# Kernel optimization log

Measured on AMD Instinct MI355X. Metric: run time of the kernel, lower is better.

The kernel has to match this reference:

```python
import jax, jax.numpy as jnp
import numpy as np

STRIDE = 2
PADDING = 1


def setup_inputs() -> dict:
    key = jax.random.key(0)
    k1, k2, k3, k4, k5 = jax.random.split(key, 5)
    B, C, H, W = 32, 128, 64, 64
    O, kh, kw = 256, 3, 3
    ah = H + 2 * PADDING - (kh - 1)  # 64
    oh = ah // STRIDE                # 32 (divisible -> ceil == floor, rest == 0)
    inputs = {
        "input": jax.random.normal(k1, (B, C, H, W), dtype=jnp.float32),
        "weight": jax.random.normal(k2, (O, C, kh, kw), dtype=jnp.float32) * 0.05,
        "bias": jax.random.normal(k3, (O,), dtype=jnp.float32) * 0.05,
        "selh": jax.random.randint(k4, (oh, oh), 0, STRIDE, dtype=jnp.int32),
        "selw": jax.random.randint(k5, (oh, oh), 0, STRIDE, dtype=jnp.int32),
    }
    return inputs


def reference(input, weight, bias, selh, selw):
    # Faithful to SConv2dAvg.forward with stoch=True, mask == -1, stride=2:
    # unfold(input, k, pad, stride=1) -> stochastic gather of one position per
    # stride x stride cell (offsets selh/selw) -> GEMM with flattened weight -> reshape.
    B, C, H, W = input.shape
    O, _, kh, kw = weight.shape
    ah = H + 2 * PADDING - (kh - 1)
    aw = W + 2 * PADDING - (kw - 1)
    oh = ah // STRIDE  # divisible by construction; ceil_mode correction is a no-op
    ow = aw // STRIDE
    xp = jnp.pad(input, ((0, 0), (0, 0), (PADDING, PADDING), (PADDING, PADDING)))
    # selected unfold positions in the afterconv grid
    rng_h = selh + (jnp.arange(oh, dtype=selh.dtype) * STRIDE)[:, None]   # [oh, ow]
    rng_w = selw + (jnp.arange(ow, dtype=selw.dtype) * STRIDE)[None, :]   # [oh, ow]
    # gather k x k patches directly (equivalent to gathering unfold columns)
    rows = rng_h[:, :, None, None] + jnp.arange(kh)[None, None, :, None]  # [oh, ow, kh, 1]
    cols = rng_w[:, :, None, None] + jnp.arange(kw)[None, None, None, :]  # [oh, ow, 1, kw]
    patches = xp[:, :, rows, cols]  # [B, C, oh, ow, kh, kw]
    out = jnp.einsum('bchwij,ocij->bohw', patches, weight) + bias[None, :, None, None]
    return out  # [B, O, oh, ow]
```

## Files before the change

### kernel.cpp

```cpp
#include <hip/hip_runtime.h>
#include <hip/hip_bf16.h>


typedef short bf16x8 __attribute__((ext_vector_type(8)));
typedef float f32x4  __attribute__((ext_vector_type(4)));

#define NSTEP 36
#define WPRE_BYTES (NSTEP * 256 * 32 * 2)
#define TRANS_BYTES (32 * 66 * 66 * 128 * 2)
#define TOTAL_WS (WPRE_BYTES + TRANS_BYTES)

__device__ __forceinline__ unsigned short f2bf(float x) {
  unsigned u = __float_as_uint(x);
  return (unsigned short)((u + 0x7fffu + ((u >> 16) & 1u)) >> 16);
}
__device__ __forceinline__ unsigned pk2(float a, float b) {
  unsigned ua = __float_as_uint(a), ub = __float_as_uint(b);
  return ((ua + 0x7fffu + ((ua >> 16) & 1u)) >> 16) |
         ((ub + 0x7fffu + ((ub >> 16) & 1u)) & 0xffff0000u);
}
__device__ __forceinline__ bf16x8 ld_frag(const uint4* a) {
  union { uint4 u; bf16x8 s; } cv; cv.u = *a; return cv.s;
}
__device__ __forceinline__ void async16(const void* g, void* l) {
  __builtin_amdgcn_global_load_lds(
      (__attribute__((address_space(1))) void*)(void*)g,
      (__attribute__((address_space(3))) void*)l, 16, 0, 0);
}

__global__ __launch_bounds__(256) void prep(const float* __restrict__ in,
                                            const float* __restrict__ w,
                                            unsigned short* __restrict__ tp,
                                            unsigned short* __restrict__ wpre) {
  const int tid = threadIdx.x;
  if (blockIdx.x >= 66) {
    const int s    = blockIdx.x - 66;
    const int o    = (blockIdx.y << 3) + (tid >> 5);
    const int k_in = tid & 31;
    const int kg   = (s << 5) + (((k_in >> 3) ^ ((o >> 1) & 3)) << 3) + (k_in & 7);
    const int tap  = kg >> 7;
    const int c    = kg & 127;
    const int di   = (tap >= 6) ? 2 : ((tap >= 3) ? 1 : 0);
    const int dj   = tap - di * 3;
    wpre[(s << 13) + (o << 5) + k_in] = f2bf(w[(o * 128 + c) * 9 + di * 3 + dj]);
    return;
  }
  __shared__ float lds[128 * 65];
  const int hp = blockIdx.x;
  const int b  = blockIdx.y;
  uint4* rowp = (uint4*)(tp + (size_t)(b * 66 + hp) * 66 * 128);
  uint4 z; z.x = z.y = z.z = z.w = 0u;
  if (hp == 0 || hp == 65) {
    for (int s = tid; s < 1056; s += 256) rowp[s] = z;
    return;
  }
  const int h = hp - 1;
  const float* src = in + ((size_t)b << 19) + (h << 6);
  const int ww4 = (tid & 15) << 2;
  const int c0  = tid >> 4;
#pragma unroll
  for (int pass = 0; pass < 8; ++pass) {
    int c = (pass << 4) + c0;
    float4 v = *(const float4*)(src + ((size_t)c << 12) + ww4);
    float* lp = lds + c * 65 + ww4;
    lp[0] = v.x; lp[1] = v.y; lp[2] = v.z; lp[3] = v.w;
  }
  __syncthreads();
  for (int s = tid; s < 1056; s += 256) {
    if (s < 16 || s >= 1040) { rowp[s] = z; continue; }
    int idx = s - 16;
    int wq = idx >> 4, c8 = idx & 15;
    const float* lp = lds + (c8 << 3) * 65 + wq;
    uint4 d;
    d.x = pk2(lp[0],   lp[65]);
    d.y = pk2(lp[130], lp[195]);
    d.z = pk2(lp[260], lp[325]);
    d.w = pk2(lp[390], lp[455]);
    rowp[s] = d;
  }
}

__global__ __launch_bounds__(256, 2) void sconv_mfma5(
    const unsigned short* __restrict__ tp,
    const unsigned short* __restrict__ wpre,
    const float* __restrict__ bias,
    const int* __restrict__ selh,
    const int* __restrict__ selw,
    float* __restrict__ out)
{
  __shared__ uint4 Alds[4][512];
  __shared__ uint4 Blds[4][512];
  __shared__ float bias_s[128];

  const int tid = threadIdx.x;
  const int d0    = blockIdx.x;
  const int blk   = ((d0 & 7) << 6) + (d0 >> 3);
  const int b     = blk >> 4;
  const int y0    = ((blk >> 1) & 7) << 2;
  const int ohalf = blk & 1;

  if (tid < 128) bias_s[tid] = bias[(ohalf << 7) + tid];

  const int wv = tid >> 6, ln = tid & 63;

  size_t asrc0, asrc1;
  {
    const int c4 = ln & 3;
#pragma unroll
    for (int r = 0; r < 2; ++r) {
      const int p  = (wv << 5) + (r << 4) + (ln >> 2);
      const int py = y0 + (p >> 5);
      const int px = p & 31;
      const int addr = (b * 66 + 2 * py + selh[(py << 5) | px]) * 66
                     + 2 * px + selw[(py << 5) | px];
      const int u = c4 ^ ((p >> 1) & 3);
      const size_t v = ((size_t)addr << 8) + (u << 4);
      if (r == 0) asrc0 = v; else asrc1 = v;
    }
  }
  const char* tbase = (const char*)tp;
  const char* wB = (const char*)wpre + (ohalf << 13) + ((wv << 1) << 10) + (ln << 4);

  const int wo = wv & 1, wp = wv >> 1;
  const int lo = ln & 15, hi = ln >> 4;

  f32x4 acc[4][4] = {};

#define STAGE(BUF, KK)                                                        \
  do {                                                                        \
    const int tap_ = (KK) >> 2;                                               \
    const int di_  = (tap_ >= 6) ? 2 : ((tap_ >= 3) ? 1 : 0);                 \
    const int dj_  = tap_ - 3 * di_;                                          \
    const int toff_ = ((di_ * 66 + dj_) << 8) + (((KK) & 3) << 6);            \
    async16(tbase + asrc0 + toff_, &Alds[BUF][(wv << 1) << 6]);               \
    async16(tbase + asrc1 + toff_, &Alds[BUF][((wv << 1) + 1) << 6]);         \
    async16(wB + ((KK) << 14),        &Blds[BUF][(wv << 1) << 6]);            \
    async16(wB + ((KK) << 14) + 1024, &Blds[BUF][((wv << 1) + 1) << 6]);      \
  } while (0)

#define DO_MMA(BUF)                                                           \
  do {                                                                        \
    const uint4* A_ = &Alds[BUF][0];                                          \
    const uint4* B_ = &Blds[BUF][0];                                          \
    bf16x8 FW[4], FP[4];                                                      \
    _Pragma("unroll")                                                         \
    for (int f = 0; f < 4; ++f) {                                             \
      const int orow = (wo << 6) + (f << 4) + lo;                             \
      FW[f] = ld_frag(B_ + (orow << 2) + (hi ^ ((orow >> 1) & 3)));           \
    }                                                                         \
    _Pragma("unroll")                                                         \
    for (int f = 0; f < 4; ++f) {                                             \
      const int prow = (wp << 6) + (f << 4) + lo;                             \
      FP[f] = ld_frag(A_ + (prow << 2) + (hi ^ ((prow >> 1) & 3)));           \
    }                                                                         \
    __builtin_amdgcn_s_setprio(1);                                            \
    _Pragma("unroll")                                                         \
    for (int fo = 0; fo < 4; ++fo)                                            \
      _Pragma("unroll")                                                       \
      for (int fp = 0; fp < 4; ++fp)                                          \
        acc[fo][fp] = __builtin_amdgcn_mfma_f32_16x16x32_bf16(                \
            FW[fo], FP[fp], acc[fo][fp], 0, 0, 0);                            \
    __builtin_amdgcn_s_setprio(0);                                            \
  } while (0)

  STAGE(0, 0);
  STAGE(1, 1);

#pragma unroll 4
  for (int kk = 0; kk < NSTEP - 2; ++kk) {
    STAGE((kk + 2) & 3, kk + 2);
    asm volatile("s_waitcnt vmcnt(8)" ::: "memory");
    __builtin_amdgcn_s_barrier();
    asm volatile("" ::: "memory");
    DO_MMA(kk & 3);
    asm volatile("s_waitcnt lgkmcnt(0)" ::: "memory");
  }

  asm volatile("s_waitcnt vmcnt(4)" ::: "memory");
  __builtin_amdgcn_s_barrier();
  asm volatile("" ::: "memory");
  DO_MMA(2);
  asm volatile("s_waitcnt lgkmcnt(0)" ::: "memory");

  asm volatile("s_waitcnt vmcnt(0)" ::: "memory");
  __builtin_amdgcn_s_barrier();
  asm volatile("" ::: "memory");
  DO_MMA(3);
#undef STAGE
#undef DO_MMA

  float* ob = out + ((size_t)b << 18) + ((size_t)ohalf << 17) + (y0 << 5);
#pragma unroll
  for (int fo = 0; fo < 4; ++fo) {
    const int obase = (wo << 6) + (fo << 4) + (hi << 2);
#pragma unroll
    for (int fp = 0; fp < 4; ++fp) {
      const int pix = (wp << 6) + (fp << 4) + lo;
#pragma unroll
      for (int j = 0; j < 4; ++j) {
        const int o = obase + j;
        ob[((size_t)o << 10) + pix] = acc[fo][fp][j] + bias_s[o];
      }
    }
  }
}

__global__ __launch_bounds__(256) void sconv_naive(
    const float* __restrict__ in, const float* __restrict__ w,
    const float* __restrict__ bias, const int* __restrict__ selh,
    const int* __restrict__ selw, float* __restrict__ out) {
  int idx = (blockIdx.x << 8) + threadIdx.x;
  if (idx >= 32 * 256 * 32 * 32) return;
  int x = idx & 31, y = (idx >> 5) & 31, o = (idx >> 10) & 255, b = idx >> 18;
  int rh0 = 2 * y + selh[(y << 5) | x] - 1;
  int rw0 = 2 * x + selw[(y << 5) | x] - 1;
  const float* inb = in + ((size_t)b << 19);
  const float* wo_ = w + o * 1152;
  float acc = bias[o];
  for (int c = 0; c < 128; ++c)
    for (int i = 0; i < 3; ++i) {
      int rh = rh0 + i;
      if (rh < 0 || rh >= 64) continue;
      for (int j = 0; j < 3; ++j) {
        int rw = rw0 + j;
        if (rw < 0 || rw >= 64) continue;
        acc += inb[(c << 12) + (rh << 6) + rw] * wo_[c * 9 + i * 3 + j];
      }
    }
  out[idx] = acc;
}

extern "C" void kernel_launch(void* const* d_in, const int* in_sizes, int n_in,
                              void* d_out, int out_size, void* d_ws, size_t ws_size,
                              hipStream_t stream) {
  const float* in   = (const float*)d_in[0];
  const float* w    = (const float*)d_in[1];
  const float* bias = (const float*)d_in[2];
  const int*   selh = (const int*)d_in[3];
  const int*   selw = (const int*)d_in[4];
  float* out = (float*)d_out;

  if (ws_size >= (size_t)TOTAL_WS) {
    unsigned short* wpre = (unsigned short*)d_ws;
    unsigned short* tp   = (unsigned short*)((char*)d_ws + WPRE_BYTES);
    prep<<<dim3(102, 32), dim3(256), 0, stream>>>(in, w, tp, wpre);
    sconv_mfma5<<<dim3(512), dim3(256), 0, stream>>>(tp, wpre, bias, selh, selw, out);
  } else {
    sconv_naive<<<dim3(32768), dim3(256), 0, stream>>>(in, w, bias, selh, selw, out);
  }
}
```

Before: 46.11 us.

## Widen conv GEMM tile to full 256 outputs with K=64 double-buffered stages

The MFMA kernel now uses 512-thread blocks that each compute all 256 output channels for 128 pixels, instead of 256-thread blocks covering half the channels. The K step grows from 32 to 64, giving 18 stages instead of 36, with two-deep double buffering and an XOR-swizzled weight layout rebuilt in prep. The aim is to halve redundant loads of the gathered input patches and cut per-step barrier overhead. In exchange the grid drops to 256 blocks at one block per CU, which lowers occupancy and leaves a shallower prefetch pipeline with an extra barrier every step.

```diff
diff --git a/kernel.cpp b/kernel.cpp
--- a/kernel.cpp
+++ b/kernel.cpp
@@ -5,8 +5,7 @@
 typedef short bf16x8 __attribute__((ext_vector_type(8)));
 typedef float f32x4  __attribute__((ext_vector_type(4)));
 
-#define NSTEP 36
-#define WPRE_BYTES (NSTEP * 256 * 32 * 2)
+#define WPRE_BYTES (18 * 256 * 64 * 2)
 #define TRANS_BYTES (32 * 66 * 66 * 128 * 2)
 #define TOTAL_WS (WPRE_BYTES + TRANS_BYTES)
 
@@ -34,15 +33,13 @@
                                             unsigned short* __restrict__ wpre) {
   const int tid = threadIdx.x;
   if (blockIdx.x >= 66) {
-    const int s    = blockIdx.x - 66;
-    const int o    = (blockIdx.y << 3) + (tid >> 5);
-    const int k_in = tid & 31;
-    const int kg   = (s << 5) + (((k_in >> 3) ^ ((o >> 1) & 3)) << 3) + (k_in & 7);
-    const int tap  = kg >> 7;
-    const int c    = kg & 127;
-    const int di   = (tap >= 6) ? 2 : ((tap >= 3) ? 1 : 0);
-    const int dj   = tap - di * 3;
-    wpre[(s << 13) + (o << 5) + k_in] = f2bf(w[(o * 128 + c) * 9 + di * 3 + dj]);
+    const int L   = ((((blockIdx.x - 66) << 5) + blockIdx.y) << 8) + tid;
+    const int e   = L & 7;
+    const int pos = (L >> 3) & 7;
+    const int o   = (L >> 6) & 255;
+    const int t   = L >> 14;
+    const int c   = ((t & 1) << 6) + ((pos ^ (o & 7)) << 3) + e;
+    wpre[L] = f2bf(w[(o * 128 + c) * 9 + (t >> 1)]);
     return;
   }
   __shared__ float lds[128 * 65];
@@ -80,7 +77,7 @@
   }
 }
 
-__global__ __launch_bounds__(256, 2) void sconv_mfma5(
+__global__ __launch_bounds__(512, 1) void sconv_mfma9(
     const unsigned short* __restrict__ tp,
     const unsigned short* __restrict__ wpre,
     const float* __restrict__ bias,
@@ -88,118 +85,117 @@
     const int* __restrict__ selw,
     float* __restrict__ out)
 {
-  __shared__ uint4 Alds[4][512];
-  __shared__ uint4 Blds[4][512];
-  __shared__ float bias_s[128];
+  __shared__ uint4 Alds[2][1024];
+  __shared__ uint4 Blds[2][2048];
+  __shared__ float bias_s[256];
 
   const int tid = threadIdx.x;
-  const int d0    = blockIdx.x;
-  const int blk   = ((d0 & 7) << 6) + (d0 >> 3);
-  const int b     = blk >> 4;
-  const int y0    = ((blk >> 1) & 7) << 2;
-  const int ohalf = blk & 1;
-
-  if (tid < 128) bias_s[tid] = bias[(ohalf << 7) + tid];
+  const int d0  = blockIdx.x;
+  const int blk = ((d0 & 7) << 5) | (d0 >> 3);
+  const int b   = blk >> 3;
+  const int y0  = (blk & 7) << 2;
+
+  if (tid < 256) bias_s[tid] = bias[tid];
 
   const int wv = tid >> 6, ln = tid & 63;
-
-  size_t asrc0, asrc1;
+  const int lo = ln & 15, hi = ln >> 4;
+
+  const int p = tid >> 2;
+  const int q = tid & 3;
+  int asrc;
   {
-    const int c4 = ln & 3;
-#pragma unroll
-    for (int r = 0; r < 2; ++r) {
-      const int p  = (wv << 5) + (r << 4) + (ln >> 2);
-      const int py = y0 + (p >> 5);
-      const int px = p & 31;
-      const int addr = (b * 66 + 2 * py + selh[(py << 5) | px]) * 66
-                     + 2 * px + selw[(py << 5) | px];
-      const int u = c4 ^ ((p >> 1) & 3);
-      const size_t v = ((size_t)addr << 8) + (u << 4);
-      if (r == 0) asrc0 = v; else asrc1 = v;
-    }
-  }
+    const int py = y0 + (p >> 5), px = p & 31;
+    asrc = (((b * 66 + 2 * py + selh[(py << 5) | px]) * 66
+             + 2 * px + selw[(py << 5) | px]) << 8);
+  }
+  const int cxor = q ^ (p & 3);
   const char* tbase = (const char*)tp;
-  const char* wB = (const char*)wpre + (ohalf << 13) + ((wv << 1) << 10) + (ln << 4);
-
-  const int wo = wv & 1, wp = wv >> 1;
-  const int lo = ln & 15, hi = ln >> 4;
+  const char* wsrc = (const char*)wpre + (((wv << 8) + ln) << 4);
+
+  const int wo = wv >> 1;
+  const int wp = wv & 1;
 
   f32x4 acc[4][4] = {};
 
-#define STAGE(BUF, KK)                                                        \
+#define STAGE(BUF, T)                                                         \
   do {                                                                        \
-    const int tap_ = (KK) >> 2;                                               \
+    const int tap_ = (T) >> 1;                                                \
     const int di_  = (tap_ >= 6) ? 2 : ((tap_ >= 3) ? 1 : 0);                 \
     const int dj_  = tap_ - 3 * di_;                                          \
-    const int toff_ = ((di_ * 66 + dj_) << 8) + (((KK) & 3) << 6);            \
-    async16(tbase + asrc0 + toff_, &Alds[BUF][(wv << 1) << 6]);               \
-    async16(tbase + asrc1 + toff_, &Alds[BUF][((wv << 1) + 1) << 6]);         \
-    async16(wB + ((KK) << 14),        &Blds[BUF][(wv << 1) << 6]);            \
-    async16(wB + ((KK) << 14) + 1024, &Blds[BUF][((wv << 1) + 1) << 6]);      \
+    const int ab_  = asrc + ((di_ * 66 + dj_) << 8) + (((T) & 1) << 7);       \
+         \
+    async16(tbase + ab_ + (cxor << 4),        &Alds[BUF][(wv << 7)]);         \
+    async16(tbase + ab_ + ((4 + cxor) << 4),  &Alds[BUF][(wv << 7) + 64]);    \
+                                                \
+    async16(wsrc + ((T) << 15),         &Blds[BUF][(wv << 8)]);               \
+    async16(wsrc + ((T) << 15) + 1024,  &Blds[BUF][(wv << 8) + 64]);          \
+    async16(wsrc + ((T) << 15) + 2048,  &Blds[BUF][(wv << 8) + 128]);         \
+    async16(wsrc + ((T) << 15) + 3072,  &Blds[BUF][(wv << 8) + 192]);         \
   } while (0)
 
-#define DO_MMA(BUF)                                                           \
+#define COMPUTE(BUF)                                                          \
   do {                                                                        \
     const uint4* A_ = &Alds[BUF][0];                                          \
     const uint4* B_ = &Blds[BUF][0];                                          \
-    bf16x8 FW[4], FP[4];                                                      \
+    bf16x8 FW[4][2], FP[4][2];                                                \
     _Pragma("unroll")                                                         \
     for (int f = 0; f < 4; ++f) {                                             \
-      const int orow = (wo << 6) + (f << 4) + lo;                             \
-      FW[f] = ld_frag(B_ + (orow << 2) + (hi ^ ((orow >> 1) & 3)));           \
-    }                                                                         \
-    _Pragma("unroll")                                                         \
-    for (int f = 0; f < 4; ++f) {                                             \
-      const int prow = (wp << 6) + (f << 4) + lo;                             \
-      FP[f] = ld_frag(A_ + (prow << 2) + (hi ^ ((prow >> 1) & 3)));           \
+      const int O = (wo << 6) + (f << 4) + lo;                                \
+      const int P = (wp << 6) + (f << 4) + lo;                                \
+      _Pragma("unroll")                                                       \
+      for (int ks = 0; ks < 2; ++ks) {                                        \
+        FW[f][ks] = ld_frag(B_ + (O << 3) + (((ks << 2) | hi) ^ (lo & 7)));   \
+        FP[f][ks] = ld_frag(A_ + ((P >> 4) << 7) + (ks << 6)                  \
+                            + ((P & 15) << 2) + (hi ^ (P & 3)));              \
+      }                                                                       \
     }                                                                         \
     __builtin_amdgcn_s_setprio(1);                                            \
     _Pragma("unroll")                                                         \
     for (int fo = 0; fo < 4; ++fo)                                            \
       _Pragma("unroll")                                                       \
       for (int fp = 0; fp < 4; ++fp)                                          \
-        acc[fo][fp] = __builtin_amdgcn_mfma_f32_16x16x32_bf16(                \
-            FW[fo], FP[fp], acc[fo][fp], 0, 0, 0);                            \
+        _Pragma("unroll")                                                     \
+        for (int ks = 0; ks < 2; ++ks)                                        \
+          acc[fo][fp] = __builtin_amdgcn_mfma_f32_16x16x32_bf16(              \
+              FW[fo][ks], FP[fp][ks], acc[fo][fp], 0, 0, 0);                  \
     __builtin_amdgcn_s_setprio(0);                                            \
   } while (0)
 
+  asm volatile("s_waitcnt vmcnt(0) lgkmcnt(0)" ::: "memory");
+  __builtin_amdgcn_s_barrier();
+  asm volatile("" ::: "memory");
+
   STAGE(0, 0);
-  STAGE(1, 1);
-
-#pragma unroll 4
-  for (int kk = 0; kk < NSTEP - 2; ++kk) {
-    STAGE((kk + 2) & 3, kk + 2);
-    asm volatile("s_waitcnt vmcnt(8)" ::: "memory");
+
+#pragma unroll
+  for (int t = 0; t < 18; ++t) {
+    if (t < 17) {
+      STAGE((t + 1) & 1, t + 1);
+      asm volatile("s_waitcnt vmcnt(6)" ::: "memory");
+    } else {
+      asm volatile("s_waitcnt vmcnt(0)" ::: "memory");
+    }
     __builtin_amdgcn_s_barrier();
     asm volatile("" ::: "memory");
-    DO_MMA(kk & 3);
+    COMPUTE(t & 1);
     asm volatile("s_waitcnt lgkmcnt(0)" ::: "memory");
-  }
-
-  asm volatile("s_waitcnt vmcnt(4)" ::: "memory");
-  __builtin_amdgcn_s_barrier();
-  asm volatile("" ::: "memory");
-  DO_MMA(2);
-  asm volatile("s_waitcnt lgkmcnt(0)" ::: "memory");
-
-  asm volatile("s_waitcnt vmcnt(0)" ::: "memory");
-  __builtin_amdgcn_s_barrier();
-  asm volatile("" ::: "memory");
-  DO_MMA(3);
+    __builtin_amdgcn_s_barrier();
+    asm volatile("" ::: "memory");
+  }
 #undef STAGE
-#undef DO_MMA
-
-  float* ob = out + ((size_t)b << 18) + ((size_t)ohalf << 17) + (y0 << 5);
+#undef COMPUTE
+
+  float* ob = out + ((size_t)b << 18) + (y0 << 5);
 #pragma unroll
   for (int fo = 0; fo < 4; ++fo) {
     const int obase = (wo << 6) + (fo << 4) + (hi << 2);
 #pragma unroll
     for (int fp = 0; fp < 4; ++fp) {
-      const int pix = (wp << 6) + (fp << 4) + lo;
+      const int P = (wp << 6) + (fp << 4) + lo;
 #pragma unroll
       for (int j = 0; j < 4; ++j) {
         const int o = obase + j;
-        ob[((size_t)o << 10) + pix] = acc[fo][fp][j] + bias_s[o];
+        ob[((size_t)o << 10) + P] = acc[fo][fp][j] + bias_s[o];
       }
     }
   }
@@ -244,7 +240,7 @@
     unsigned short* wpre = (unsigned short*)d_ws;
     unsigned short* tp   = (unsigned short*)((char*)d_ws + WPRE_BYTES);
     prep<<<dim3(102, 32), dim3(256), 0, stream>>>(in, w, tp, wpre);
-    sconv_mfma5<<<dim3(512), dim3(256), 0, stream>>>(tp, wpre, bias, selh, selw, out);
+    sconv_mfma9<<<dim3(256), dim3(512), 0, stream>>>(tp, wpre, bias, selh, selw, out);
   } else {
     sconv_naive<<<dim3(32768), dim3(256), 0, stream>>>(in, w, bias, selh, selw, out);
   }
```

Result: slower. 51.58 us (+11.9%).
